# Kernel tuning notes

Measured on AMD Instinct MI355X. Metric: run time of the kernel, lower is better.

Reference implementation:

```python
import jax, jax.numpy as jnp
import numpy as np

N_HEADS = 16

def setup_inputs() -> dict:
    key = jax.random.key(0)
    ks = jax.random.split(key, 6)
    B, S, D = 2, 2048, 1024
    sc = 0.02
    return {
        "x": jax.random.normal(ks[0], (B, S, D), dtype=jnp.float32),
        "Wq": jax.random.normal(ks[1], (D, D), dtype=jnp.float32) * sc,
        "Wk": jax.random.normal(ks[2], (D, D), dtype=jnp.float32) * sc,
        "Wv": jax.random.normal(ks[3], (D, D), dtype=jnp.float32) * sc,
        "Wo": jax.random.normal(ks[4], (D, D), dtype=jnp.float32) * sc,
        "bo": jnp.zeros((D,), dtype=jnp.float32),
        "stride": 64,
    }

def _strided_mask(S: int, stride: int):
    # local window |i-j|<=1  OR  |i-j| == k*stride (k>=1); diff==0 is in the window
    i = jnp.arange(S)[:, None]
    j = jnp.arange(S)[None, :]
    diff = jnp.abs(i - j)
    return (diff <= 1) | (diff % stride == 0)  # [S, S] bool

def reference(x, Wq, Wk, Wv, Wo, bo, stride):
    B, S, D = x.shape
    H = N_HEADS
    Dh = D // H
    # q/k/v projections: nn.Linear(bias=False) applies x @ W.T
    def proj(W):
        return (x @ W.T).reshape(B, S, H, Dh).transpose(0, 2, 1, 3)  # [B,H,S,Dh]
    q, k, v = proj(Wq), proj(Wk), proj(Wv)
    scores = jnp.einsum('bhqd,bhkd->bhqk', q, k) / jnp.sqrt(jnp.float32(Dh))
    mask = _strided_mask(S, stride)  # [S,S]
    scores = jnp.where(mask[None, None], scores, -jnp.inf)
    attn = jax.nn.softmax(scores, axis=-1)  # dropout is identity in eval
    out = jnp.einsum('bhqk,bhkd->bhqd', attn, v)  # [B,H,S,Dh]
    out = out.transpose(0, 2, 1, 3).reshape(B, S, D)
    return out @ Wo.T + bo
```

## Files before the change

kernel.cpp:

```cpp
#include <hip/hip_runtime.h>
#include <hip/hip_bf16.h>


typedef __bf16 bf16;
typedef __attribute__((ext_vector_type(4))) __bf16 bf16x4;
typedef __attribute__((ext_vector_type(8))) __bf16 bf16x8;
typedef __attribute__((ext_vector_type(4))) float f32x4;
typedef __attribute__((ext_vector_type(4))) unsigned int u32x4;

constexpr int S_ = 2048;
constexpr int D_ = 1024;
constexpr int H_ = 16;
constexpr int DH = 64;
constexpr int M_ = 2 * S_;

__device__ __forceinline__ void gload_lds16(const bf16* g, bf16* l) {
    __builtin_amdgcn_global_load_lds(
        (const __attribute__((address_space(1))) void*)g,
        (__attribute__((address_space(3))) void*)l, 16, 0, 0);
}

#define BARRIER_FULL() do { asm volatile("" ::: "memory"); \
    __builtin_amdgcn_sched_barrier(0); \
    __builtin_amdgcn_s_barrier(); \
    __builtin_amdgcn_sched_barrier(0); \
    asm volatile("" ::: "memory"); } while (0)

#define WAIT_LGKM0() do { asm volatile("s_waitcnt lgkmcnt(0)" ::: "memory"); \
    __builtin_amdgcn_sched_barrier(0); } while (0)

#define WAIT_VM0() do { asm volatile("s_waitcnt vmcnt(0)" ::: "memory"); \
    __builtin_amdgcn_sched_barrier(0); } while (0)

#define WAIT_VM4() do { asm volatile("s_waitcnt vmcnt(4)" ::: "memory"); \
    __builtin_amdgcn_sched_barrier(0); } while (0)

__device__ __forceinline__ void stage32(const bf16* __restrict__ G, int base_row,
                                        int kcol, bf16* lds, int wave, int lane)
{
    const int rIn = lane >> 2;
    const int g   = (lane & 3) ^ ((lane >> 2) & 3) ^ (lane >> 4);
    #pragma unroll
    for (int l = 0; l < 2; ++l) {
        const int R = (wave * 2 + l) * 16;
        gload_lds16(G + (size_t)(base_row + R + rIn) * D_ + kcol + g * 8,
                    lds + R * 32);
    }
}

__global__ __launch_bounds__(512, 1)
void gemm_qkv_p2(const bf16* __restrict__ A,
                 const bf16* __restrict__ W,
                 bf16* __restrict__ C)
{
    constexpr int BK = 32;
    constexpr int NT = D_ / BK;
    constexpr int TSLOT = 256 * BK;
    __shared__ __align__(16) bf16 As[3 * TSLOT];
    __shared__ __align__(16) bf16 Bs[3 * TSLOT];

    const int tid  = threadIdx.x;
    const int wave = tid >> 6;
    const int lane = tid & 63;
    const int wm = wave >> 2;
    const int wn = wave & 3;

    const int lid = blockIdx.y * 12 + blockIdx.x;
    const int xcd = lid & 7, pos = lid >> 3;
    const int bxs = (xcd & 1) * 6 + pos % 6;
    const int bys = (xcd >> 1) * 4 + pos / 6;
    const int bm = bys * 256;
    const int bn = bxs * 256;

    const int l15 = lane & 15;
    const int rs  = (lane >> 4) ^ (lane & 3) ^ ((lane >> 2) & 3);
    const int aRd = wm * 4096 + l15 * 32 + rs * 8;
    const int bRd = wn * 2048 + l15 * 32 + rs * 8;

    f32x4 acc[8][4];
    #pragma unroll
    for (int i = 0; i < 8; ++i)
        #pragma unroll
        for (int j = 0; j < 4; ++j) acc[i][j] = f32x4{0.f, 0.f, 0.f, 0.f};

    bf16x8 aF[4], bF[4];

#define READA_HALF(H) do { _Pragma("unroll") \
    for (int fm = 0; fm < 4; ++fm) \
        aF[fm] = *(const bf16x8*)(aslot + aRd + (H) * 2048 + fm * 512); \
    } while (0)

#define READB_ALL() do { _Pragma("unroll") \
    for (int fn = 0; fn < 4; ++fn) \
        bF[fn] = *(const bf16x8*)(bslot + bRd + fn * 512); \
    } while (0)

#define MFMA16(H) do { _Pragma("unroll") \
    for (int fm = 0; fm < 4; ++fm) { _Pragma("unroll") \
        for (int fn = 0; fn < 4; ++fn) \
            acc[(H) * 4 + fm][fn] = __builtin_amdgcn_mfma_f32_16x16x32_bf16( \
                aF[fm], bF[fn], acc[(H) * 4 + fm][fn], 0, 0, 0); \
    } } while (0)

    stage32(A, bm, 0,  As,         wave, lane);
    stage32(W, bn, 0,  Bs,         wave, lane);
    stage32(A, bm, BK, As + TSLOT, wave, lane);
    stage32(W, bn, BK, Bs + TSLOT, wave, lane);
    WAIT_VM4();
    BARRIER_FULL();

    int cur = 0;
    for (int t = 0; t < NT; ++t) {
        const int ss = (cur + 2 >= 3) ? (cur - 1) : (cur + 2);
        const bf16* aslot = As + cur * TSLOT;
        const bf16* bslot = Bs + cur * TSLOT;
        const bool pre = (t + 2) < NT;
        const int kn = (t + 2) * BK;

        READB_ALL();
        READA_HALF(0);
        if (pre) stage32(A, bm, kn, As + ss * TSLOT, wave, lane);
        BARRIER_FULL(); WAIT_LGKM0();
        __builtin_amdgcn_s_setprio(1); MFMA16(0); __builtin_amdgcn_s_setprio(0);
        BARRIER_FULL();

        READA_HALF(1);
        if (pre) stage32(W, bn, kn, Bs + ss * TSLOT, wave, lane);
        BARRIER_FULL(); WAIT_LGKM0();
        __builtin_amdgcn_s_setprio(1); MFMA16(1); __builtin_amdgcn_s_setprio(0);
        WAIT_VM4();
        BARRIER_FULL();

        cur = (cur + 1 >= 3) ? 0 : (cur + 1);
    }
#undef READA_HALF
#undef READB_ALL
#undef MFMA16

    #pragma unroll
    for (int fm8 = 0; fm8 < 8; ++fm8) {
        #pragma unroll
        for (int fn4 = 0; fn4 < 4; ++fn4) {
            const int n = bn + wn * 64 + fn4 * 16 + l15;
            const int z = n >> 10, col = n & 1023;
            bf16* Cz = C + (size_t)z * M_ * D_;
            const int mb = bm + wm * 128 + fm8 * 16 + (lane >> 4) * 4;
            #pragma unroll
            for (int r2 = 0; r2 < 4; ++r2)
                Cz[(size_t)(mb + r2) * D_ + col] = (bf16)acc[fm8][fn4][r2];
        }
    }
}

template<bool AF32, bool BF32, bool CF32, bool BIAS>
__global__ __launch_bounds__(256)
void gemm_bt(const void* __restrict__ Av,
             const void* __restrict__ W0v, const void* __restrict__ W1v,
             const void* __restrict__ W2v,
             void* __restrict__ Cv, const float* __restrict__ bias)
{
    constexpr int BM = 128, BK = 64;
    constexpr int N = D_, K = D_;
    __shared__ __align__(16) bf16 As[BM * BK];
    __shared__ __align__(16) bf16 Bs[BM * BK];

    const int z = blockIdx.z;
    const void* Wv_ = (z == 0) ? W0v : (z == 1) ? W1v : W2v;

    const int tid  = threadIdx.x;
    const int wave = tid >> 6;
    const int lane = tid & 63;

    int bxs = blockIdx.x, bys = blockIdx.y;
    if (gridDim.z == 1 && gridDim.x == 8 && gridDim.y == 32) {
        const int lid = blockIdx.y * 8 + blockIdx.x;
        const int xcd = lid & 7, pos = lid >> 3;
        bxs = pos & 7;
        bys = xcd * 4 + (pos >> 3);
    }
    const int bm = bys * BM;
    const int bn = bxs * BM;
    const int wr = wave >> 1;
    const int wc = wave & 1;

    f32x4 acc[4][4];
    #pragma unroll
    for (int i = 0; i < 4; ++i)
        #pragma unroll
        for (int j = 0; j < 4; ++j)
            acc[i][j] = f32x4{0.f, 0.f, 0.f, 0.f};

    const int ldRow = lane >> 3;
    const int ldCol = (lane & 7) * 8;

    for (int kt = 0; kt < K; kt += BK) {
        if (AF32) {
            const float* A = (const float*)Av;
            #pragma unroll
            for (int it = 0; it < 8; ++it) {
                const int flat = (it * 256 + tid) * 4;
                const int row = flat >> 6, col = flat & 63;
                const float4 v = *(const float4*)(A + (size_t)(bm + row) * K + kt + col);
                bf16x4 p = { (bf16)v.x, (bf16)v.y, (bf16)v.z, (bf16)v.w };
                *(bf16x4*)&As[row * BK + col] = p;
            }
        } else {
            const bf16* A = (const bf16*)Av;
            #pragma unroll
            for (int q = 0; q < 4; ++q) {
                const int c = wave * 4 + q;
                const int row = c * 8 + ldRow;
                gload_lds16(A + (size_t)(bm + row) * K + kt + ldCol, &As[c * 8 * BK]);
            }
        }
        if (BF32) {
            const float* W = (const float*)Wv_;
            #pragma unroll
            for (int it = 0; it < 8; ++it) {
                const int flat = (it * 256 + tid) * 4;
                const int row = flat >> 6, col = flat & 63;
                const float4 v = *(const float4*)(W + (size_t)(bn + row) * K + kt + col);
                bf16x4 p = { (bf16)v.x, (bf16)v.y, (bf16)v.z, (bf16)v.w };
                *(bf16x4*)&Bs[row * BK + col] = p;
            }
        } else {
            const bf16* W = (const bf16*)Wv_;
            #pragma unroll
            for (int q = 0; q < 4; ++q) {
                const int c = wave * 4 + q;
                const int row = c * 8 + ldRow;
                gload_lds16(W + (size_t)(bn + row) * K + kt + ldCol, &Bs[c * 8 * BK]);
            }
        }
        __syncthreads();
        #pragma unroll
        for (int kk = 0; kk < 2; ++kk) {
            const int k0 = kk * 32 + (lane >> 4) * 8;
            bf16x8 af[4], bfv[4];
            #pragma unroll
            for (int mi = 0; mi < 4; ++mi)
                af[mi] = *(const bf16x8*)&As[(wr * 64 + mi * 16 + (lane & 15)) * BK + k0];
            #pragma unroll
            for (int ni = 0; ni < 4; ++ni)
                bfv[ni] = *(const bf16x8*)&Bs[(wc * 64 + ni * 16 + (lane & 15)) * BK + k0];
            #pragma unroll
            for (int mi = 0; mi < 4; ++mi)
                #pragma unroll
                for (int ni = 0; ni < 4; ++ni)
                    acc[mi][ni] = __builtin_amdgcn_mfma_f32_16x16x32_bf16(
                        af[mi], bfv[ni], acc[mi][ni], 0, 0, 0);
        }
        __syncthreads();
    }

    #pragma unroll
    for (int mi = 0; mi < 4; ++mi) {
        #pragma unroll
        for (int ni = 0; ni < 4; ++ni) {
            const int n  = bn + wc * 64 + ni * 16 + (lane & 15);
            const int mb = bm + wr * 64 + mi * 16 + (lane >> 4) * 4;
            float bv = 0.f;
            if (BIAS) bv = bias[n];
            #pragma unroll
            for (int r2 = 0; r2 < 4; ++r2) {
                const int m = mb + r2;
                if (CF32) {
                    ((float*)Cv)[(size_t)m * N + n] = acc[mi][ni][r2] + bv;
                } else {
                    bf16* Cc = (bf16*)Cv + (size_t)z * M_ * D_;
                    Cc[(size_t)m * N + n] = (bf16)(acc[mi][ni][r2] + bv);
                }
            }
        }
    }
}

__global__ __launch_bounds__(256)
void convert_to_bf16(const float* __restrict__ x,
                     const float* __restrict__ w0, const float* __restrict__ w1,
                     const float* __restrict__ w2, const float* __restrict__ w3,
                     bf16* __restrict__ out)
{
    const size_t eid = ((size_t)blockIdx.x * 256 + threadIdx.x) * 8;
    const float* src; size_t off;
    if (eid < (size_t)(1u << 22)) { src = x; off = eid; }
    else {
        const size_t t = eid - (1u << 22);
        const int k = (int)(t >> 20);
        off = t & ((1u << 20) - 1);
        src = (k == 0) ? w0 : (k == 1) ? w1 : (k == 2) ? w2 : w3;
    }
    const float4 a = *(const float4*)(src + off);
    const float4 c = *(const float4*)(src + off + 4);
    bf16x8 v = { (bf16)a.x, (bf16)a.y, (bf16)a.z, (bf16)a.w,
                 (bf16)c.x, (bf16)c.y, (bf16)c.z, (bf16)c.w };
    *(bf16x8*)(out + eid) = v;
}

__device__ __forceinline__ unsigned pk2bf(float lo, float hi) {
    const unsigned a = __builtin_bit_cast(unsigned short, (bf16)lo);
    const unsigned b = __builtin_bit_cast(unsigned short, (bf16)hi);
    return a | (b << 16);
}

__global__ __launch_bounds__(256)
void attn_mfma(bf16* __restrict__ QA, const bf16* __restrict__ Kw,
               const bf16* __restrict__ Vw)
{
    const int lane = threadIdx.x & 63;
    const int wid  = blockIdx.x * 4 + (threadIdx.x >> 6);
    const int r = wid & 63;
    const int h = (wid >> 6) & (H_ - 1);
    const int b = wid >> 10;

    const int qlo = lane & 15;
    const int g   = lane >> 4;
    const size_t rb = (size_t)b * S_;
    const int col0 = h * DH;
    const float scale = 0.125f;

    f32x4 accS[2][2];
    #pragma unroll
    for (int a = 0; a < 2; ++a)
        #pragma unroll
        for (int c = 0; c < 2; ++c) accS[a][c] = f32x4{0.f,0.f,0.f,0.f};

    #pragma unroll
    for (int c = 0; c < 2; ++c) {
        bf16x8 kf[2], qf[2];
        #pragma unroll
        for (int t = 0; t < 2; ++t) {
            const size_t row = rb + (size_t)(r + 64 * (t * 16 + qlo));
            kf[t] = *(const bf16x8*)&Kw[row * D_ + col0 + c * 32 + g * 8];
            qf[t] = *(const bf16x8*)&QA[row * D_ + col0 + c * 32 + g * 8];
        }
        #pragma unroll
        for (int kt = 0; kt < 2; ++kt)
            #pragma unroll
            for (int qt = 0; qt < 2; ++qt)
                accS[kt][qt] = __builtin_amdgcn_mfma_f32_16x16x32_bf16(
                    kf[kt], qf[qt], accS[kt][qt], 0, 0, 0);
    }

    const int s_nb = lane & 31;
    const int side = lane >> 5;
    const int i_nb = r + 64 * s_nb;
    const int j_nb = side ? (i_nb + 1) : (i_nb - 1);
    const bool nbv = (unsigned)j_nb < (unsigned)S_;
    const int j_sf = nbv ? j_nb : i_nb;
    float nbd = 0.f;
    #pragma unroll
    for (int t = 0; t < 8; ++t) {
        const bf16x8 qv = *(const bf16x8*)&QA[(rb + i_nb) * D_ + col0 + t * 8];
        const bf16x8 kv = *(const bf16x8*)&Kw[(rb + j_sf) * D_ + col0 + t * 8];
        #pragma unroll
        for (int e = 0; e < 8; ++e) nbd += (float)qv[e] * (float)kv[e];
    }
    const float NEGINF = -__builtin_inff();
    float nb = nbv ? nbd * scale : NEGINF;

    float mx[2] = { NEGINF, NEGINF };
    #pragma unroll
    for (int kt = 0; kt < 2; ++kt)
        #pragma unroll
        for (int qt = 0; qt < 2; ++qt)
            #pragma unroll
            for (int rr = 0; rr < 4; ++rr)
                mx[qt] = fmaxf(mx[qt], accS[kt][qt][rr]);
    mx[0] *= scale; mx[1] *= scale;
    mx[g & 1] = fmaxf(mx[g & 1], nb);
    #pragma unroll
    for (int x = 16; x <= 32; x <<= 1) {
        mx[0] = fmaxf(mx[0], __shfl_xor(mx[0], x));
        mx[1] = fmaxf(mx[1], __shfl_xor(mx[1], x));
    }
    float p[2][2][4];
    float sm[2] = { 0.f, 0.f };
    #pragma unroll
    for (int kt = 0; kt < 2; ++kt)
        #pragma unroll
        for (int qt = 0; qt < 2; ++qt)
            #pragma unroll
            for (int rr = 0; rr < 4; ++rr) {
                const float e = __expf(accS[kt][qt][rr] * scale - mx[qt]);
                p[kt][qt][rr] = e;
                sm[qt] += e;
            }
    float nbp = __expf(nb - mx[g & 1]);
    sm[g & 1] += nbp;
    #pragma unroll
    for (int x = 16; x <= 32; x <<= 1) {
        sm[0] += __shfl_xor(sm[0], x);
        sm[1] += __shfl_xor(sm[1], x);
    }
    const float inv[2] = { 1.f / sm[0], 1.f / sm[1] };
    #pragma unroll
    for (int kt = 0; kt < 2; ++kt)
        #pragma unroll
        for (int qt = 0; qt < 2; ++qt)
            #pragma unroll
            for (int rr = 0; rr < 4; ++rr) p[kt][qt][rr] *= inv[qt];
    nbp *= inv[g & 1];

    unsigned pk_[2][2][2];
    #pragma unroll
    for (int qt = 0; qt < 2; ++qt)
        #pragma unroll
        for (int kt = 0; kt < 2; ++kt)
            #pragma unroll
            for (int w = 0; w < 2; ++w)
                pk_[qt][kt][w] = pk2bf(p[kt][qt][2 * w], p[kt][qt][2 * w + 1]);

    const int srcA = qlo + 32 * (g & 1);
    const int srcB = srcA + 16;
    const int kts  = g >> 1;
    bf16x8 pa[2];
    #pragma unroll
    for (int qt = 0; qt < 2; ++qt) {
        u32x4 fr;
        #pragma unroll
        for (int w = 0; w < 2; ++w) {
            const unsigned a0 = (unsigned)__shfl((int)pk_[qt][0][w], srcA);
            const unsigned a1 = (unsigned)__shfl((int)pk_[qt][1][w], srcA);
            fr[w] = kts ? a1 : a0;
            const unsigned b0 = (unsigned)__shfl((int)pk_[qt][0][w], srcB);
            const unsigned b1 = (unsigned)__shfl((int)pk_[qt][1][w], srcB);
            fr[2 + w] = kts ? b1 : b0;
        }
        pa[qt] = __builtin_bit_cast(bf16x8, fr);
    }

    f32x4 accO[2][4];
    #pragma unroll
    for (int qt = 0; qt < 2; ++qt)
        #pragma unroll
        for (int dt = 0; dt < 4; ++dt) accO[qt][dt] = f32x4{0.f,0.f,0.f,0.f};
    #pragma unroll
    for (int dt = 0; dt < 4; ++dt) {
        bf16x8 vf;
        #pragma unroll
        for (int e = 0; e < 8; ++e)
            vf[e] = Vw[(rb + (size_t)(r + 64 * (g * 8 + e))) * D_ + col0 + dt * 16 + qlo];
        accO[0][dt] = __builtin_amdgcn_mfma_f32_16x16x32_bf16(pa[0], vf, accO[0][dt], 0, 0, 0);
        accO[1][dt] = __builtin_amdgcn_mfma_f32_16x16x32_bf16(pa[1], vf, accO[1][dt], 0, 0, 0);
    }

    #pragma unroll
    for (int qt = 0; qt < 2; ++qt)
        #pragma unroll
        for (int rr = 0; rr < 4; ++rr) {
            const int q  = qt * 16 + g * 4 + rr;
            const int iq = r + 64 * q;
            const float pm = __shfl(nbp, q);
            const float pp = __shfl(nbp, q + 32);
            const int jm = iq > 0 ? iq - 1 : 0;
            const int jp = iq < S_ - 1 ? iq + 1 : S_ - 1;
            #pragma unroll
            for (int dt = 0; dt < 4; ++dt) {
                const int d = col0 + dt * 16 + qlo;
                const float vm = (float)Vw[(rb + jm) * D_ + d];
                const float vp = (float)Vw[(rb + jp) * D_ + d];
                const float o = accO[qt][dt][rr] + pm * vm + pp * vp;
                QA[(rb + iq) * D_ + d] = (bf16)o;
            }
        }
}

extern "C" void kernel_launch(void* const* d_in, const int* in_sizes, int n_in,
                              void* d_out, int out_size, void* d_ws, size_t ws_size,
                              hipStream_t stream)
{
    const float* x  = (const float*)d_in[0];
    const float* Wq = (const float*)d_in[1];
    const float* Wk = (const float*)d_in[2];
    const float* Wv = (const float*)d_in[3];
    const float* Wo = (const float*)d_in[4];
    const float* bo = (const float*)d_in[5];

    bf16* qws = (bf16*)d_ws;
    bf16* kws = qws + (size_t)M_ * D_;
    bf16* vws = kws + (size_t)M_ * D_;

    const bool fast = ws_size >= (size_t)40 * 1024 * 1024;

    if (fast) {
        bf16* xb  = vws + (size_t)M_ * D_;
        bf16* wqb = xb + (1u << 22);
        bf16* wob = wqb + 3 * (1u << 20);

        convert_to_bf16<<<4096, 256, 0, stream>>>(x, Wq, Wk, Wv, Wo, xb);

        gemm_qkv_p2<<<dim3(3 * D_ / 256, M_ / 256), 512, 0, stream>>>(xb, wqb, qws);

        attn_mfma<<<dim3(2 * H_ * 64 / 4), 256, 0, stream>>>(qws, kws, vws);

        gemm_bt<false, false, true, true><<<dim3(D_/128, M_/128, 1), 256, 0, stream>>>(
            qws, wob, nullptr, nullptr, (float*)d_out, bo);
    } else {
        gemm_bt<true, true, false, false><<<dim3(D_/128, M_/128, 3), 256, 0, stream>>>(
            x, Wq, Wk, Wv, qws, nullptr);

        attn_mfma<<<dim3(2 * H_ * 64 / 4), 256, 0, stream>>>(qws, kws, vws);

        gemm_bt<false, true, true, true><<<dim3(D_/128, M_/128, 1), 256, 0, stream>>>(
            qws, Wo, nullptr, nullptr, (float*)d_out, bo);
    }
}
```

Measured before the change: 93.79 us.

## Simplify QKV GEMM pipeline to one barrier per step and add pipelined O-projection GEMM

The QKV GEMM loop now issues both A and W prefetches up front, then runs LDS reads and MFMAs for both halves with a single barrier per K-step instead of four. Launch bounds are raised to allow two blocks per CU. A new triple-buffered, direct-to-LDS 128x128 output-projection GEMM with XCD-aware block remapping replaces the generic gemm_bt for the Wo stage. The goal is less synchronisation overhead and a faster final GEMM. The risks are register pressure under the tighter launch bound and LDS read/write hazards now guarded only by a single barrier.

```diff
diff --git a/kernel.cpp b/kernel.cpp
--- a/kernel.cpp
+++ b/kernel.cpp
@@ -26,9 +26,6 @@
     __builtin_amdgcn_sched_barrier(0); \
     asm volatile("" ::: "memory"); } while (0)
 
-#define WAIT_LGKM0() do { asm volatile("s_waitcnt lgkmcnt(0)" ::: "memory"); \
-    __builtin_amdgcn_sched_barrier(0); } while (0)
-
 #define WAIT_VM0() do { asm volatile("s_waitcnt vmcnt(0)" ::: "memory"); \
     __builtin_amdgcn_sched_barrier(0); } while (0)
 
@@ -48,7 +45,7 @@
     }
 }
 
-__global__ __launch_bounds__(512, 1)
+__global__ __launch_bounds__(512, 2)
 void gemm_qkv_p2(const bf16* __restrict__ A,
                  const bf16* __restrict__ W,
                  bf16* __restrict__ C)
@@ -85,23 +82,6 @@
 
     bf16x8 aF[4], bF[4];
 
-#define READA_HALF(H) do { _Pragma("unroll") \
-    for (int fm = 0; fm < 4; ++fm) \
-        aF[fm] = *(const bf16x8*)(aslot + aRd + (H) * 2048 + fm * 512); \
-    } while (0)
-
-#define READB_ALL() do { _Pragma("unroll") \
-    for (int fn = 0; fn < 4; ++fn) \
-        bF[fn] = *(const bf16x8*)(bslot + bRd + fn * 512); \
-    } while (0)
-
-#define MFMA16(H) do { _Pragma("unroll") \
-    for (int fm = 0; fm < 4; ++fm) { _Pragma("unroll") \
-        for (int fn = 0; fn < 4; ++fn) \
-            acc[(H) * 4 + fm][fn] = __builtin_amdgcn_mfma_f32_16x16x32_bf16( \
-                aF[fm], bF[fn], acc[(H) * 4 + fm][fn], 0, 0, 0); \
-    } } while (0)
-
     stage32(A, bm, 0,  As,         wave, lane);
     stage32(W, bn, 0,  Bs,         wave, lane);
     stage32(A, bm, BK, As + TSLOT, wave, lane);
@@ -115,27 +95,43 @@
         const bf16* aslot = As + cur * TSLOT;
         const bf16* bslot = Bs + cur * TSLOT;
         const bool pre = (t + 2) < NT;
-        const int kn = (t + 2) * BK;
-
-        READB_ALL();
-        READA_HALF(0);
-        if (pre) stage32(A, bm, kn, As + ss * TSLOT, wave, lane);
-        BARRIER_FULL(); WAIT_LGKM0();
-        __builtin_amdgcn_s_setprio(1); MFMA16(0); __builtin_amdgcn_s_setprio(0);
+
+        if (pre) {
+            const int kn = (t + 2) * BK;
+            stage32(A, bm, kn, As + ss * TSLOT, wave, lane);
+            stage32(W, bn, kn, Bs + ss * TSLOT, wave, lane);
+        }
+
+        #pragma unroll
+        for (int fn = 0; fn < 4; ++fn)
+            bF[fn] = *(const bf16x8*)(bslot + bRd + fn * 512);
+        #pragma unroll
+        for (int fm = 0; fm < 4; ++fm)
+            aF[fm] = *(const bf16x8*)(aslot + aRd + fm * 512);
+        __builtin_amdgcn_s_setprio(1);
+        #pragma unroll
+        for (int fm = 0; fm < 4; ++fm)
+            #pragma unroll
+            for (int fn = 0; fn < 4; ++fn)
+                acc[fm][fn] = __builtin_amdgcn_mfma_f32_16x16x32_bf16(
+                    aF[fm], bF[fn], acc[fm][fn], 0, 0, 0);
+        __builtin_amdgcn_s_setprio(0);
+        #pragma unroll
+        for (int fm = 0; fm < 4; ++fm)
+            aF[fm] = *(const bf16x8*)(aslot + aRd + 2048 + fm * 512);
+        __builtin_amdgcn_s_setprio(1);
+        #pragma unroll
+        for (int fm = 0; fm < 4; ++fm)
+            #pragma unroll
+            for (int fn = 0; fn < 4; ++fn)
+                acc[4 + fm][fn] = __builtin_amdgcn_mfma_f32_16x16x32_bf16(
+                    aF[fm], bF[fn], acc[4 + fm][fn], 0, 0, 0);
+        __builtin_amdgcn_s_setprio(0);
+
+        if (pre) { WAIT_VM4(); } else { WAIT_VM0(); }
         BARRIER_FULL();
-
-        READA_HALF(1);
-        if (pre) stage32(W, bn, kn, Bs + ss * TSLOT, wave, lane);
-        BARRIER_FULL(); WAIT_LGKM0();
-        __builtin_amdgcn_s_setprio(1); MFMA16(1); __builtin_amdgcn_s_setprio(0);
-        WAIT_VM4();
-        BARRIER_FULL();
-
         cur = (cur + 1 >= 3) ? 0 : (cur + 1);
     }
-#undef READA_HALF
-#undef READB_ALL
-#undef MFMA16
 
     #pragma unroll
     for (int fm8 = 0; fm8 < 8; ++fm8) {
@@ -148,6 +144,97 @@
             #pragma unroll
             for (int r2 = 0; r2 < 4; ++r2)
                 Cz[(size_t)(mb + r2) * D_ + col] = (bf16)acc[fm8][fn4][r2];
+        }
+    }
+}
+
+__global__ __launch_bounds__(256)
+void gemm_o_p2(const bf16* __restrict__ A,
+               const bf16* __restrict__ W,
+               float* __restrict__ Cf,
+               const float* __restrict__ bias)
+{
+    constexpr int BK = 32;
+    constexpr int NT = D_ / BK;
+    constexpr int TSLOT = 128 * BK;
+    __shared__ __align__(16) bf16 As[3 * TSLOT];
+    __shared__ __align__(16) bf16 Bs[3 * TSLOT];
+
+    const int tid  = threadIdx.x;
+    const int wave = tid >> 6;
+    const int lane = tid & 63;
+    const int wm = wave >> 1;
+    const int wn = wave & 1;
+
+    const int lid = blockIdx.y * 8 + blockIdx.x;
+    const int xcd = lid & 7, pos = lid >> 3;
+    const int bxs = (xcd & 3) * 2 + (pos & 1);
+    const int bys = (xcd >> 2) * 16 + (pos >> 1);
+    const int bm = bys * 128;
+    const int bn = bxs * 128;
+
+    const int l15 = lane & 15;
+    const int rs  = (lane >> 4) ^ (lane & 3) ^ ((lane >> 2) & 3);
+    const int aRd = wm * 2048 + l15 * 32 + rs * 8;
+    const int bRd = wn * 2048 + l15 * 32 + rs * 8;
+
+    f32x4 acc[4][4];
+    #pragma unroll
+    for (int i = 0; i < 4; ++i)
+        #pragma unroll
+        for (int j = 0; j < 4; ++j) acc[i][j] = f32x4{0.f, 0.f, 0.f, 0.f};
+
+    bf16x8 aF[4], bF[4];
+
+    stage32(A, bm, 0,  As,         wave, lane);
+    stage32(W, bn, 0,  Bs,         wave, lane);
+    stage32(A, bm, BK, As + TSLOT, wave, lane);
+    stage32(W, bn, BK, Bs + TSLOT, wave, lane);
+    WAIT_VM4();
+    BARRIER_FULL();
+
+    int cur = 0;
+    for (int t = 0; t < NT; ++t) {
+        const int ss = (cur + 2 >= 3) ? (cur - 1) : (cur + 2);
+        const bf16* aslot = As + cur * TSLOT;
+        const bf16* bslot = Bs + cur * TSLOT;
+        const bool pre = (t + 2) < NT;
+
+        if (pre) {
+            const int kn = (t + 2) * BK;
+            stage32(A, bm, kn, As + ss * TSLOT, wave, lane);
+            stage32(W, bn, kn, Bs + ss * TSLOT, wave, lane);
+        }
+        #pragma unroll
+        for (int fn = 0; fn < 4; ++fn)
+            bF[fn] = *(const bf16x8*)(bslot + bRd + fn * 512);
+        #pragma unroll
+        for (int fm = 0; fm < 4; ++fm)
+            aF[fm] = *(const bf16x8*)(aslot + aRd + fm * 512);
+        __builtin_amdgcn_s_setprio(1);
+        #pragma unroll
+        for (int fm = 0; fm < 4; ++fm)
+            #pragma unroll
+            for (int fn = 0; fn < 4; ++fn)
+                acc[fm][fn] = __builtin_amdgcn_mfma_f32_16x16x32_bf16(
+                    aF[fm], bF[fn], acc[fm][fn], 0, 0, 0);
+        __builtin_amdgcn_s_setprio(0);
+
+        if (pre) { WAIT_VM4(); } else { WAIT_VM0(); }
+        BARRIER_FULL();
+        cur = (cur + 1 >= 3) ? 0 : (cur + 1);
+    }
+
+    #pragma unroll
+    for (int fm = 0; fm < 4; ++fm) {
+        #pragma unroll
+        for (int fn = 0; fn < 4; ++fn) {
+            const int n = bn + wn * 64 + fn * 16 + l15;
+            const float bv = bias[n];
+            const int mb = bm + wm * 64 + fm * 16 + (lane >> 4) * 4;
+            #pragma unroll
+            for (int r2 = 0; r2 < 4; ++r2)
+                Cf[(size_t)(mb + r2) * D_ + n] = acc[fm][fn][r2] + bv;
         }
     }
 }
@@ -494,8 +581,8 @@
 
         attn_mfma<<<dim3(2 * H_ * 64 / 4), 256, 0, stream>>>(qws, kws, vws);
 
-        gemm_bt<false, false, true, true><<<dim3(D_/128, M_/128, 1), 256, 0, stream>>>(
-            qws, wob, nullptr, nullptr, (float*)d_out, bo);
+        gemm_o_p2<<<dim3(D_ / 128, M_ / 128), 256, 0, stream>>>(
+            qws, wob, (float*)d_out, bo);
     } else {
         gemm_bt<true, true, false, false><<<dim3(D_/128, M_/128, 3), 256, 0, stream>>>(
             x, Wq, Wk, Wv, qws, nullptr);
```

Result: slower. 103.1 us (+9.9%).
